# Kernel optimization log

Hardware: AMD Instinct MI355X
Metric: run time of the kernel (lower is better)

The kernel has to match this reference:

```python
import jax, jax.numpy as jnp
import numpy as np

B, S, N, SD = 1024, 8, 64, 36
EPS = 1e-5

def _lrelu(x):
    return jnp.where(x > 0, x, 0.01 * x)

def _inorm(x, g, b):
    # x: [B,S,N,C]; InstanceNorm(axis=3) on a [1,1,N,C] tensor normalizes over N per channel
    mu = jnp.mean(x, axis=2, keepdims=True)
    var = jnp.var(x, axis=2, keepdims=True)
    return (x - mu) * jax.lax.rsqrt(var + EPS) * g + b

def _conv1d_same(x, w, b):
    # x: [B,S,Cin], w: [K,Cin,Cout]; TF 'same' even-kernel pads (0, k-1-pl)
    k = w.shape[0]
    pl = (k - 1) // 2
    y = jax.lax.conv_general_dilated(x, w, (1,), [(pl, k - 1 - pl)],
                                     dimension_numbers=('NWC', 'WIO', 'NWC'))
    return y + b

def setup_inputs() -> dict:
    key = jax.random.key(0)
    ks = iter(jax.random.split(key, 64))
    d = {}
    d['fts'] = jax.random.normal(next(ks), (B, S, N, 5), jnp.float32)
    d['state'] = jax.random.normal(next(ks), (B, S, SD), jnp.float32)
    def w(shape, scale=0.05):
        return jax.random.normal(next(ks), shape, jnp.float32) * scale
    # pointnet (1x1 Conv2D == pointwise matmul)
    d['pw1'] = w((5, 32)); d['pb1'] = jnp.zeros((32,)); d['pg1'] = jnp.ones((32,)); d['pbe1'] = jnp.zeros((32,))
    d['pw2'] = w((32, 64)); d['pb2'] = jnp.zeros((64,)); d['pg2'] = jnp.ones((64,)); d['pbe2'] = jnp.zeros((64,))
    d['pw3'] = w((64, 128)); d['pb3'] = jnp.zeros((128,)); d['pg3'] = jnp.ones((128,)); d['pbe3'] = jnp.zeros((128,))
    d['pw4'] = w((128, 128)); d['pb4'] = jnp.zeros((128,))
    # fts_mergenet Conv1D stack + Dense
    d['mw1'] = w((2, 128, 128)); d['mb1'] = jnp.zeros((128,))
    d['mw2'] = w((2, 128, 64)); d['mb2'] = jnp.zeros((64,))
    d['mw3'] = w((2, 64, 64)); d['mb3'] = jnp.zeros((64,))
    d['mw4'] = w((2, 64, 64)); d['mb4'] = jnp.zeros((64,))
    d['mdw'] = w((S * 64, 128)); d['mdb'] = jnp.zeros((128,))
    # states_conv Conv1D stack + Dense
    d['sw1'] = w((2, SD, 128)); d['sb1'] = jnp.zeros((128,))
    d['sw2'] = w((2, 128, 64)); d['sb2'] = jnp.zeros((64,))
    d['sw3'] = w((2, 64, 64)); d['sb3'] = jnp.zeros((64,))
    d['sw4'] = w((2, 64, 64)); d['sb4'] = jnp.zeros((64,))
    d['sdw'] = w((S * 64, 128)); d['sdb'] = jnp.zeros((128,))
    # control module Dense stack
    d['cw1'] = w((256, 128)); d['cb1'] = jnp.zeros((128,))
    d['cw2'] = w((128, 64)); d['cb2'] = jnp.zeros((64,))
    d['cw3'] = w((64, 32)); d['cb3'] = jnp.zeros((32,))
    d['cw4'] = w((32, 4)); d['cb4'] = jnp.zeros((4,))
    return d

def reference(fts, state, pw1, pb1, pg1, pbe1, pw2, pb2, pg2, pbe2,
              pw3, pb3, pg3, pbe3, pw4, pb4,
              mw1, mb1, mw2, mb2, mw3, mb3, mw4, mb4, mdw, mdb,
              sw1, sb1, sw2, sb2, sw3, sb3, sw4, sb4, sdw, sdb,
              cw1, cb1, cw2, cb2, cw3, cb3, cw4, cb4):
    # --- pointnet, fully batched over (B,S) instead of tf.map_fn per timestep ---
    x = fts  # [B,S,N,5]
    x = _lrelu(_inorm(jnp.einsum('bsnc,cd->bsnd', x, pw1) + pb1, pg1, pbe1))
    x = _lrelu(_inorm(jnp.einsum('bsnc,cd->bsnd', x, pw2) + pb2, pg2, pbe2))
    x = _lrelu(_inorm(jnp.einsum('bsnc,cd->bsnd', x, pw3) + pb3, pg3, pbe3))
    x = jnp.einsum('bsnc,cd->bsnd', x, pw4) + pb4
    emb = jnp.mean(x, axis=2)  # GlobalAveragePooling2D over (1,N) -> [B,S,128]
    # --- fts_mergenet ---
    y = _lrelu(_conv1d_same(emb, mw1, mb1))
    y = _lrelu(_conv1d_same(y, mw2, mb2))
    y = _lrelu(_conv1d_same(y, mw3, mb3))
    y = _lrelu(_conv1d_same(y, mw4, mb4))
    fts_emb = y.reshape(y.shape[0], -1) @ mdw + mdb  # [B,128]
    # --- states branch ---
    z = _lrelu(_conv1d_same(state, sw1, sb1))
    z = _lrelu(_conv1d_same(z, sw2, sb2))
    z = _lrelu(_conv1d_same(z, sw3, sb3))
    z = _conv1d_same(z, sw4, sb4)  # no activation after 4th conv
    st_emb = z.reshape(z.shape[0], -1) @ sdw + sdb  # [B,128]
    # --- control head ---
    t = jnp.concatenate([fts_emb, st_emb], axis=1)  # [B,256]
    t = _lrelu(t @ cw1 + cb1)
    t = _lrelu(t @ cw2 + cb2)
    t = _lrelu(t @ cw3 + cb3)
    out = t @ cw4 + cb4  # [B,4]
    thrust = jax.nn.sigmoid(out[:, :1])
    body = jnp.tanh(out[:, 1:])
    mult = jnp.array([21.0, 6.0, 6.0, 6.0], dtype=out.dtype)
    return jnp.concatenate([thrust, body], axis=1) * mult
```

## Files before the change

kernel.cpp:

```cpp
#include <hip/hip_runtime.h>
#include <hip/hip_bf16.h>
#include <math.h>

#define THREADS 256

constexpr int S   = 8;
constexpr int NPT = 64;
constexpr int SD  = 36;
constexpr float EPS = 1e-5f;

typedef float v4f __attribute__((ext_vector_type(4)));
typedef __attribute__((ext_vector_type(8))) short bf8;
typedef __attribute__((ext_vector_type(4))) float f4;

__device__ __forceinline__ float lrelu(float x) { return fmaxf(x, 0.01f * x); }

__device__ __forceinline__ unsigned short f2bf(float x) {
  return __builtin_bit_cast(unsigned short, __float2bfloat16(x));
}

__device__ __forceinline__ void pack_frag(const float* __restrict__ src, unsigned short* __restrict__ dst,
                                          int slot, int NT, int TS, int CIN, int N) {
  const int f = slot >> 6, l = slot & 63;
  const int nt = f % NT, kt = f / NT;
  const int n = nt * 16 + (l & 15), g = (l >> 4);
  unsigned short* d = dst + (size_t)f * 512 + l * 8;
#pragma unroll
  for (int j = 0; j < 8; ++j) {
    int k = kt * 32 + g * 8 + j;
    float v;
    if (TS > 0) { int tap = k / TS, c = k - tap * TS; v = (c < CIN) ? src[(tap * CIN + c) * N + n] : 0.f; }
    else        v = (CIN == 0 || k < CIN) ? src[k * N + n] : 0.f;
    d[j] = f2bf(v);
  }
}

__device__ __forceinline__ void pack_frag_fold(const float* __restrict__ pw4,
    const float* __restrict__ mw1, unsigned short* __restrict__ dst, int slot) {
  const int f = slot >> 6, l = slot & 63;
  const int nt = f & 7, kt = f >> 3;
  const int n = nt * 16 + (l & 15), g = l >> 4;
  const int k0 = kt * 32 + g * 8;
  const int tap = k0 >> 7, c0 = k0 & 127;
  float acc[8] = {};
  const float* mcol = mw1 + (size_t)tap * 128 * 128 + n;
  const float* pr   = pw4 + (size_t)c0 * 128;
  for (int d = 0; d < 128; ++d) {
    float m = mcol[(size_t)d * 128];
#pragma unroll
    for (int j = 0; j < 8; ++j) acc[j] = fmaf(pr[j * 128 + d], m, acc[j]);
  }
  unsigned short* dd = dst + (size_t)f * 512 + l * 8;
#pragma unroll
  for (int j = 0; j < 8; ++j) dd[j] = f2bf(acc[j]);
}

#define WOFF_PNW1 0
#define WOFF_PNW2 1024
#define WOFF_PNW3 3072
#define WOFF_MW1  11264
#define WOFF_MW2  44032
#define WOFF_MW3  60416
#define WOFF_MW4  68608
#define WOFF_MDW  76800
#define WOFF_SW1  142336
#define WOFF_SW2  154624
#define WOFF_SW3  171008
#define WOFF_SW4  179200
#define WOFF_SDW  187392

__global__ void prep_weights(const float* __restrict__ pw1, const float* __restrict__ pw2,
    const float* __restrict__ pw3,
    const float* __restrict__ pw4, const float* __restrict__ pb4,
    const float* __restrict__ mw1, const float* __restrict__ mb1,
    const float* __restrict__ mw2, const float* __restrict__ mw3,
    const float* __restrict__ mw4, const float* __restrict__ mdw,
    const float* __restrict__ sw1, const float* __restrict__ sw2, const float* __restrict__ sw3,
    const float* __restrict__ sw4, const float* __restrict__ sdw,
    unsigned short* __restrict__ wf, float* __restrict__ mb1p, float* __restrict__ mb1p7) {
  const int slot = blockIdx.x * 256 + threadIdx.x;
  if      (slot <   128) pack_frag(pw1,    wf + WOFF_PNW1, slot,          2,   0,   5,  32);
  else if (slot <   384) pack_frag(pw2,    wf + WOFF_PNW2, slot - 128,    4,   0,   0,  64);
  else if (slot <  1408) pack_frag(pw3,    wf + WOFF_PNW3, slot - 384,    8,   0,   0, 128);
  else if (slot <  5504) pack_frag_fold(pw4, mw1, wf + WOFF_MW1, slot - 1408);
  else if (slot <  7552) pack_frag(mw2,    wf + WOFF_MW2,  slot - 5504,   4, 128, 128,  64);
  else if (slot <  8576) pack_frag(mw3,    wf + WOFF_MW3,  slot - 7552,   4,  64,  64,  64);
  else if (slot <  9600) pack_frag(mw4,    wf + WOFF_MW4,  slot - 8576,   4,  64,  64,  64);
  else if (slot < 17792) pack_frag(mdw,    wf + WOFF_MDW,  slot - 9600,   8,   0,   0, 128);
  else if (slot < 19328) pack_frag(sw1,    wf + WOFF_SW1,  slot - 17792,  8,  48,  36, 128);
  else if (slot < 21376) pack_frag(sw2,    wf + WOFF_SW2,  slot - 19328,  4, 128, 128,  64);
  else if (slot < 22400) pack_frag(sw3,    wf + WOFF_SW3,  slot - 21376,  4,  64,  64,  64);
  else if (slot < 23424) pack_frag(sw4,    wf + WOFF_SW4,  slot - 22400,  4,  64,  64,  64);
  else if (slot < 31616) pack_frag(sdw,    wf + WOFF_SDW,  slot - 23424,  8,   0,   0, 128);
  else if (slot < 31744) {
    const int n = slot - 31616;
    float a = mb1[n];
    for (int d = 0; d < 128; ++d)
      a = fmaf(pb4[d], mw1[(size_t)d * 128 + n] + mw1[(size_t)(128 + d) * 128 + n], a);
    mb1p[n] = a;
  } else if (slot < 31872) {
    const int n = slot - 31744;
    float a = mb1[n];
    for (int d = 0; d < 128; ++d) a = fmaf(pb4[d], mw1[(size_t)d * 128 + n], a);
    mb1p7[n] = a;
  }
}

__global__ __launch_bounds__(THREADS)
void pointnet_kernel(const float* __restrict__ fts,
    const unsigned short* __restrict__ w1f, const float* __restrict__ pg1, const float* __restrict__ pbe1,
    const unsigned short* __restrict__ w2f, const float* __restrict__ pg2, const float* __restrict__ pbe2,
    const unsigned short* __restrict__ w3f, const float* __restrict__ pg3, const float* __restrict__ pbe3,
    unsigned short* __restrict__ xbar_out)
{
  const int p = blockIdx.x;
  const int t = threadIdx.x;
  const int l = t & 63, w = t >> 6;
  const int g = l >> 4, lc = l & 15;

  __shared__ unsigned short xinb[64 * 40];
  __shared__ unsigned short x1b[64 * 40];
  __shared__ unsigned short x2b[64 * 72];

  {
    const float* src = fts + (size_t)p * 320;
    unsigned* xz = (unsigned*)xinb;
    const int row = t >> 2, cp = t & 3;
    const float* sr = src + row * 5;
    unsigned v0 = 0u;
    if (cp == 0)      v0 = (unsigned)f2bf(sr[0]) | ((unsigned)f2bf(sr[1]) << 16);
    else if (cp == 1) v0 = (unsigned)f2bf(sr[2]) | ((unsigned)f2bf(sr[3]) << 16);
    else if (cp == 2) v0 = (unsigned)f2bf(sr[4]);
    unsigned* xr = xz + row * 20;
    xr[cp]      = v0;
    xr[cp + 4]  = 0u;
    xr[cp + 8]  = 0u;
    xr[cp + 12] = 0u;
  }
  __syncthreads();

  if (w < 2) {
    f4 c1[4];
#pragma unroll
    for (int mt = 0; mt < 4; ++mt) c1[mt] = f4{0.f, 0.f, 0.f, 0.f};
    bf8 bfrag = *(const bf8*)(w1f + ((size_t)w * 64 + l) * 8);
#pragma unroll
    for (int mt = 0; mt < 4; ++mt) {
      bf8 afrag = *(const bf8*)(xinb + (mt * 16 + lc) * 40 + g * 8);
      c1[mt] = __builtin_amdgcn_mfma_f32_16x16x32_bf16(afrag, bfrag, c1[mt], 0, 0, 0);
    }
    float s = 0.f, q = 0.f;
#pragma unroll
    for (int mt = 0; mt < 4; ++mt)
#pragma unroll
      for (int r = 0; r < 4; ++r) { float v = c1[mt][r]; s += v; q = fmaf(v, v, q); }
    s += __shfl_xor(s, 16, 64); s += __shfl_xor(s, 32, 64);
    q += __shfl_xor(q, 16, 64); q += __shfl_xor(q, 32, 64);
    const int ch = w * 16 + lc;
    float mu  = s * (1.f / NPT);
    float inv = rsqrtf(q * (1.f / NPT) - mu * mu + EPS);
    float a = inv * pg1[ch];
    float bb = fmaf(-mu, a, pbe1[ch]);
#pragma unroll
    for (int mt = 0; mt < 4; ++mt)
#pragma unroll
      for (int r = 0; r < 4; ++r) {
        int row = mt * 16 + g * 4 + r;
        x1b[row * 40 + ch] = f2bf(lrelu(fmaf(c1[mt][r], a, bb)));
      }
  }
  __syncthreads();

  f4 c2[4];
#pragma unroll
  for (int mt = 0; mt < 4; ++mt) c2[mt] = f4{0.f, 0.f, 0.f, 0.f};
  {
    bf8 bfrag = *(const bf8*)(w2f + ((size_t)w * 64 + l) * 8);
#pragma unroll
    for (int mt = 0; mt < 4; ++mt) {
      bf8 afrag = *(const bf8*)(x1b + (mt * 16 + lc) * 40 + g * 8);
      c2[mt] = __builtin_amdgcn_mfma_f32_16x16x32_bf16(afrag, bfrag, c2[mt], 0, 0, 0);
    }
  }
  {
    float s = 0.f, q = 0.f;
#pragma unroll
    for (int mt = 0; mt < 4; ++mt)
#pragma unroll
      for (int r = 0; r < 4; ++r) { float v = c2[mt][r]; s += v; q = fmaf(v, v, q); }
    s += __shfl_xor(s, 16, 64); s += __shfl_xor(s, 32, 64);
    q += __shfl_xor(q, 16, 64); q += __shfl_xor(q, 32, 64);
    const int ch = w * 16 + lc;
    float mu  = s * (1.f / NPT);
    float inv = rsqrtf(q * (1.f / NPT) - mu * mu + EPS);
    float a = inv * pg2[ch];
    float bb = fmaf(-mu, a, pbe2[ch]);
#pragma unroll
    for (int mt = 0; mt < 4; ++mt)
#pragma unroll
      for (int r = 0; r < 4; ++r) {
        int row = mt * 16 + g * 4 + r;
        x2b[row * 72 + ch] = f2bf(lrelu(fmaf(c2[mt][r], a, bb)));
      }
  }
  __syncthreads();

  f4 c3[4][2];
#pragma unroll
  for (int mt = 0; mt < 4; ++mt)
#pragma unroll
    for (int n = 0; n < 2; ++n) c3[mt][n] = f4{0.f, 0.f, 0.f, 0.f};
  bf8 bf3[2][2];
#pragma unroll
  for (int ntl = 0; ntl < 2; ++ntl)
#pragma unroll
    for (int kt = 0; kt < 2; ++kt)
      bf3[ntl][kt] = *(const bf8*)(w3f + ((size_t)(kt * 8 + (2 * w + ntl)) * 64 + l) * 8);
#pragma unroll
  for (int mt = 0; mt < 4; ++mt)
#pragma unroll
    for (int kt = 0; kt < 2; ++kt) {
      bf8 afrag = *(const bf8*)(x2b + (mt * 16 + lc) * 72 + kt * 32 + g * 8);
#pragma unroll
      for (int ntl = 0; ntl < 2; ++ntl)
        c3[mt][ntl] = __builtin_amdgcn_mfma_f32_16x16x32_bf16(afrag, bf3[ntl][kt], c3[mt][ntl], 0, 0, 0);
    }

#pragma unroll
  for (int ntl = 0; ntl < 2; ++ntl) {
    float s = 0.f, q = 0.f;
#pragma unroll
    for (int mt = 0; mt < 4; ++mt)
#pragma unroll
      for (int r = 0; r < 4; ++r) { float v = c3[mt][ntl][r]; s += v; q = fmaf(v, v, q); }
    s += __shfl_xor(s, 16, 64); s += __shfl_xor(s, 32, 64);
    q += __shfl_xor(q, 16, 64); q += __shfl_xor(q, 32, 64);
    const int ch = w * 32 + ntl * 16 + lc;
    float mu  = s * (1.f / NPT);
    float inv = rsqrtf(q * (1.f / NPT) - mu * mu + EPS);
    float a = inv * pg3[ch];
    float bb = fmaf(-mu, a, pbe3[ch]);
    float m = 0.f;
#pragma unroll
    for (int mt = 0; mt < 4; ++mt)
#pragma unroll
      for (int r = 0; r < 4; ++r) m += lrelu(fmaf(c3[mt][ntl][r], a, bb));
    m += __shfl_xor(m, 16, 64); m += __shfl_xor(m, 32, 64);
    if (g == 0) xbar_out[(size_t)p * 128 + ch] = f2bf(m * (1.f / NPT));
  }
}

template<int KT, int NT, int TS, int SPI, int SPO, bool ACT>
__device__ __forceinline__ void mfma_conv(const unsigned short* __restrict__ xin,
    unsigned short* __restrict__ xout, const unsigned short* __restrict__ wfr,
    const float* __restrict__ bias, const float* __restrict__ bias7, int w, int l) {
  const int g = l >> 4, lc = l & 15;
  const int arow = w * 16 + lc, abl = arow >> 3, an = arow & 7;
  f4 acc[NT];
#pragma unroll
  for (int nt = 0; nt < NT; ++nt) acc[nt] = f4{0.f, 0.f, 0.f, 0.f};
#pragma unroll
  for (int kt = 0; kt < KT; ++kt) {
    const int k0 = kt * 32 + g * 8;
    const int tap = k0 / TS, c = k0 - tap * TS;
    bf8 a = *(const bf8*)(xin + (abl * 9 + an + tap) * SPI + c);
#pragma unroll
    for (int nt = 0; nt < NT; ++nt) {
      bf8 b = *(const bf8*)(wfr + ((size_t)(kt * NT + nt) * 64 + l) * 8);
      acc[nt] = __builtin_amdgcn_mfma_f32_16x16x32_bf16(a, b, acc[nt], 0, 0, 0);
    }
  }
  const int orow0 = w * 16 + g * 4;
#pragma unroll
  for (int nt = 0; nt < NT; ++nt) {
    const float bv  = bias[nt * 16 + lc];
    const float bv7 = bias7[nt * 16 + lc];
#pragma unroll
    for (int r = 0; r < 4; ++r) {
      const int rr = orow0 + r, obl = rr >> 3, on = rr & 7;
      float v = acc[nt][r] + (on == 7 ? bv7 : bv);
      if (ACT) v = lrelu(v);
      xout[(obl * 9 + on) * SPO + nt * 16 + lc] = f2bf(v);
    }
  }
}

__device__ __forceinline__ void mfma_dense512(const unsigned short* __restrict__ xin,
    float* __restrict__ P, const unsigned short* __restrict__ wfr, int w, int l) {
  const int g = l >> 4, lc = l & 15;
  const int bl = lc & 7;
  f4 acc[8];
#pragma unroll
  for (int nt = 0; nt < 8; ++nt) acc[nt] = f4{0.f, 0.f, 0.f, 0.f};
#pragma unroll
  for (int kt2 = 0; kt2 < 4; ++kt2) {
    const int kt = w * 4 + kt2;
    const int k0 = kt * 32 + g * 8;
    const int n = k0 >> 6, c = k0 & 63;
    bf8 a = *(const bf8*)(xin + (bl * 9 + n) * 72 + c);
#pragma unroll
    for (int nt = 0; nt < 8; ++nt) {
      bf8 b = *(const bf8*)(wfr + ((size_t)(kt * 8 + nt) * 64 + l) * 8);
      acc[nt] = __builtin_amdgcn_mfma_f32_16x16x32_bf16(a, b, acc[nt], 0, 0, 0);
    }
  }
  if (g < 2) {
#pragma unroll
    for (int nt = 0; nt < 8; ++nt)
#pragma unroll
      for (int r = 0; r < 4; ++r) {
        const int rr = g * 4 + r;
        P[(w * 8 + rr) * 128 + nt * 16 + lc] = acc[nt][r];
      }
  }
}

__global__ __launch_bounds__(THREADS)
void tail_mfma_kernel(const unsigned short* __restrict__ xbar, const float* __restrict__ state,
    const unsigned short* __restrict__ wf,
    const float* __restrict__ mb1p, const float* __restrict__ mb1p7,
    const float* __restrict__ mb2, const float* __restrict__ mb3,
    const float* __restrict__ mb4, const float* __restrict__ mdb,
    const float* __restrict__ sb1, const float* __restrict__ sb2, const float* __restrict__ sb3,
    const float* __restrict__ sb4, const float* __restrict__ sdb,
    float* __restrict__ femb, float* __restrict__ semb)
{
  const int t = threadIdx.x, l = t & 63, w = t >> 6;
  const bool merge = blockIdx.x < 128;
  const int bg = merge ? blockIdx.x : blockIdx.x - 128;

  __shared__ unsigned short lds[24768];
  unsigned short* BufX = lds;
  unsigned short* BufY = lds + 9792;
  unsigned short* BufZ = lds + 19584;

  { unsigned* z = (unsigned*)BufX; for (int i = t; i < 4896; i += THREADS) z[i] = 0; }
  for (int i = t; i < 8 * 136; i += THREADS) BufY[((i / 136) * 9 + 8) * 136 + (i % 136)] = 0;
  for (int i = t; i < 8 * 72;  i += THREADS) BufZ[((i / 72)  * 9 + 8) * 72  + (i % 72)]  = 0;

  if (merge) {
    for (int i = t; i < 1024; i += THREADS) {
      int bl = i >> 7, rem = i & 127, n = rem >> 4, sl = rem & 15;
      bf8 v = *(const bf8*)(xbar + (size_t)((bg * 8 + bl) * 8 + n) * 128 + sl * 8);
      *(bf8*)(BufX + (bl * 9 + n) * 136 + sl * 8) = v;
    }
  } else {
    for (int i = t; i < 2304; i += THREADS) {
      int bl = i / 288, rem = i % 288, n = rem / 36, c = rem % 36;
      BufX[(bl * 9 + n) * 48 + c] = f2bf(state[((size_t)(bg * 8 + bl) * 8 + n) * 36 + c]);
    }
  }
  __syncthreads();

  if (merge) mfma_conv<8, 8, 128, 136, 136, true>(BufX, BufY, wf + WOFF_MW1, mb1p, mb1p7, w, l);
  else       mfma_conv<3, 8,  48,  48, 136, true>(BufX, BufY, wf + WOFF_SW1, sb1, sb1, w, l);
  __syncthreads();
  if (merge) mfma_conv<8, 4, 128, 136, 72, true>(BufY, BufZ, wf + WOFF_MW2, mb2, mb2, w, l);
  else       mfma_conv<8, 4, 128, 136, 72, true>(BufY, BufZ, wf + WOFF_SW2, sb2, sb2, w, l);
  __syncthreads();
  for (int i = t; i < 8 * 72; i += THREADS) BufX[((i / 72) * 9 + 8) * 72 + (i % 72)] = 0;
  __syncthreads();
  if (merge) mfma_conv<4, 4, 64, 72, 72, true>(BufZ, BufX, wf + WOFF_MW3, mb3, mb3, w, l);
  else       mfma_conv<4, 4, 64, 72, 72, true>(BufZ, BufX, wf + WOFF_SW3, sb3, sb3, w, l);
  __syncthreads();
  if (merge) mfma_conv<4, 4, 64, 72, 72, true >(BufX, BufY, wf + WOFF_MW4, mb4, mb4, w, l);
  else       mfma_conv<4, 4, 64, 72, 72, false>(BufX, BufY, wf + WOFF_SW4, sb4, sb4, w, l);
  __syncthreads();

  float* P = (float*)lds;
  mfma_dense512(BufY, P, wf + (merge ? WOFF_MDW : WOFF_SDW), w, l);
  __syncthreads();

  const float* bias = merge ? mdb : sdb;
  float* outg = (merge ? femb : semb) + (size_t)bg * 1024;
  for (int i = t; i < 1024; i += THREADS) {
    int ch = i & 127, b = i >> 7;
    outg[i] = bias[ch] + P[(0 * 8 + b) * 128 + ch] + P[(1 * 8 + b) * 128 + ch]
                       + P[(2 * 8 + b) * 128 + ch] + P[(3 * 8 + b) * 128 + ch];
  }
}

template<int CIN, int COUT, bool ACT>
__device__ __forceinline__ void wave_dense(const float* __restrict__ in, float* __restrict__ out,
                                           const float* __restrict__ W, const float* __restrict__ bias, int l) {
  if constexpr (COUT >= 64) {
    constexpr int NC = COUT / 64;
    const int d0 = l * NC;
    float acc[NC];
#pragma unroll
    for (int k = 0; k < NC; ++k) acc[k] = bias[d0 + k];
#pragma unroll 4
    for (int c4 = 0; c4 < CIN / 4; ++c4) {
      v4f x4 = *(const v4f*)(in + 4 * c4);
#pragma unroll
      for (int j = 0; j < 4; ++j) {
        const float* wr = W + (4 * c4 + j) * COUT + d0;
#pragma unroll
        for (int k = 0; k < NC; ++k) acc[k] = fmaf(x4[j], wr[k], acc[k]);
      }
    }
#pragma unroll
    for (int k = 0; k < NC; ++k) out[d0 + k] = ACT ? lrelu(acc[k]) : acc[k];
  } else {
    if (l < COUT) {
      float acc = bias[l];
#pragma unroll 4
      for (int c4 = 0; c4 < CIN / 4; ++c4) {
        v4f x4 = *(const v4f*)(in + 4 * c4);
#pragma unroll
        for (int j = 0; j < 4; ++j) acc = fmaf(x4[j], W[(4 * c4 + j) * COUT + l], acc);
      }
      out[l] = ACT ? lrelu(acc) : acc;
    }
  }
}

__global__ __launch_bounds__(THREADS)
void head_kernel(const float* __restrict__ femb, const float* __restrict__ semb,
    const float* __restrict__ cw1, const float* __restrict__ cb1,
    const float* __restrict__ cw2, const float* __restrict__ cb2,
    const float* __restrict__ cw3, const float* __restrict__ cb3,
    const float* __restrict__ cw4, const float* __restrict__ cb4,
    float* __restrict__ out)
{
  const int t = threadIdx.x, l = t & 63, w = t >> 6;
  const int b = blockIdx.x * 4 + w;
  __shared__ float cat[4][256];
  __shared__ float hb[4][232];

  cat[w][l]       = femb[(size_t)b * 128 + l];
  cat[w][64 + l]  = femb[(size_t)b * 128 + 64 + l];
  cat[w][128 + l] = semb[(size_t)b * 128 + l];
  cat[w][192 + l] = semb[(size_t)b * 128 + 64 + l];
  __syncthreads();
  wave_dense<256, 128, true>(cat[w], hb[w], cw1, cb1, l);
  __syncthreads();
  wave_dense<128, 64, true>(hb[w], hb[w] + 128, cw2, cb2, l);
  __syncthreads();
  wave_dense<64, 32, true>(hb[w] + 128, hb[w] + 192, cw3, cb3, l);
  __syncthreads();
  if (l < 4) {
    float acc = cb4[l];
#pragma unroll
    for (int c = 0; c < 32; ++c) acc = fmaf(hb[w][192 + c], cw4[c * 4 + l], acc);
    out[(size_t)b * 4 + l] = (l == 0) ? 21.f / (1.f + expf(-acc)) : 6.f * tanhf(acc);
  }
}

extern "C" void kernel_launch(void* const* d_in, const int* in_sizes, int n_in,
                              void* d_out, int out_size, void* d_ws, size_t ws_size,
                              hipStream_t stream) {
  const float* p[44];
  for (int i = 0; i < 44; ++i) p[i] = (const float*)d_in[i];

  unsigned short* xbar_bf = (unsigned short*)d_ws;
  float* femb  = (float*)((char*)d_ws + 2097152);
  float* semb  = (float*)((char*)d_ws + 2621440);
  unsigned short* wf = (unsigned short*)((char*)d_ws + 3145728);
  float* mb1p  = (float*)((char*)d_ws + 3651584);
  float* mb1p7 = (float*)((char*)d_ws + 3652096);

  prep_weights<<<125, THREADS, 0, stream>>>(
      p[2], p[6], p[10],
      p[14], p[15], p[16], p[17],
      p[18], p[20], p[22], p[24],
      p[26], p[28], p[30], p[32], p[34],
      wf, mb1p, mb1p7);

  pointnet_kernel<<<1024 * S, THREADS, 0, stream>>>(
      p[0],
      wf + WOFF_PNW1, p[4], p[5],
      wf + WOFF_PNW2, p[8], p[9],
      wf + WOFF_PNW3, p[12], p[13],
      xbar_bf);

  tail_mfma_kernel<<<256, THREADS, 0, stream>>>(
      xbar_bf, p[1], wf,
      mb1p, mb1p7, p[19], p[21], p[23], p[25],
      p[27], p[29], p[31], p[33], p[35],
      femb, semb);

  head_kernel<<<256, THREADS, 0, stream>>>(
      femb, semb,
      p[36], p[37], p[38], p[39], p[40], p[41], p[42], p[43],
      (float*)d_out);
}
```

Before: 79.26 us.

## Fuse tail conv stacks with control head and hoist pointnet weight loads

```diff
diff --git a/kernel.cpp b/kernel.cpp
--- a/kernel.cpp
+++ b/kernel.cpp
@@ -43,12 +43,19 @@
   const int k0 = kt * 32 + g * 8;
   const int tap = k0 >> 7, c0 = k0 & 127;
   float acc[8] = {};
-  const float* mcol = mw1 + (size_t)tap * 128 * 128 + n;
-  const float* pr   = pw4 + (size_t)c0 * 128;
-  for (int d = 0; d < 128; ++d) {
-    float m = mcol[(size_t)d * 128];
-#pragma unroll
-    for (int j = 0; j < 8; ++j) acc[j] = fmaf(pr[j * 128 + d], m, acc[j]);
+  const float* mcol  = mw1 + (size_t)tap * 128 * 128 + n;
+  const float* pbase = pw4 + (size_t)c0 * 128;
+  for (int d4 = 0; d4 < 32; ++d4) {
+    const int d0 = 4 * d4;
+    float m0 = mcol[(size_t)(d0 + 0) * 128];
+    float m1 = mcol[(size_t)(d0 + 1) * 128];
+    float m2 = mcol[(size_t)(d0 + 2) * 128];
+    float m3 = mcol[(size_t)(d0 + 3) * 128];
+#pragma unroll
+    for (int j = 0; j < 8; ++j) {
+      v4f pv = *(const v4f*)(pbase + j * 128 + d0);
+      acc[j] = fmaf(pv[0], m0, fmaf(pv[1], m1, fmaf(pv[2], m2, fmaf(pv[3], m3, acc[j]))));
+    }
   }
   unsigned short* dd = dst + (size_t)f * 512 + l * 8;
 #pragma unroll
@@ -122,6 +129,16 @@
   __shared__ unsigned short x1b[64 * 40];
   __shared__ unsigned short x2b[64 * 72];
 
+  bf8 bfrag_w1 = {};
+  if (w < 2) bfrag_w1 = *(const bf8*)(w1f + ((size_t)w * 64 + l) * 8);
+  bf8 bfrag_w2 = *(const bf8*)(w2f + ((size_t)w * 64 + l) * 8);
+  bf8 bf3[2][2];
+#pragma unroll
+  for (int ntl = 0; ntl < 2; ++ntl)
+#pragma unroll
+    for (int kt = 0; kt < 2; ++kt)
+      bf3[ntl][kt] = *(const bf8*)(w3f + ((size_t)(kt * 8 + (2 * w + ntl)) * 64 + l) * 8);
+
   {
     const float* src = fts + (size_t)p * 320;
     unsigned* xz = (unsigned*)xinb;
@@ -143,11 +160,10 @@
     f4 c1[4];
 #pragma unroll
     for (int mt = 0; mt < 4; ++mt) c1[mt] = f4{0.f, 0.f, 0.f, 0.f};
-    bf8 bfrag = *(const bf8*)(w1f + ((size_t)w * 64 + l) * 8);
 #pragma unroll
     for (int mt = 0; mt < 4; ++mt) {
       bf8 afrag = *(const bf8*)(xinb + (mt * 16 + lc) * 40 + g * 8);
-      c1[mt] = __builtin_amdgcn_mfma_f32_16x16x32_bf16(afrag, bfrag, c1[mt], 0, 0, 0);
+      c1[mt] = __builtin_amdgcn_mfma_f32_16x16x32_bf16(afrag, bfrag_w1, c1[mt], 0, 0, 0);
     }
     float s = 0.f, q = 0.f;
 #pragma unroll
@@ -174,13 +190,10 @@
   f4 c2[4];
 #pragma unroll
   for (int mt = 0; mt < 4; ++mt) c2[mt] = f4{0.f, 0.f, 0.f, 0.f};
-  {
-    bf8 bfrag = *(const bf8*)(w2f + ((size_t)w * 64 + l) * 8);
-#pragma unroll
-    for (int mt = 0; mt < 4; ++mt) {
-      bf8 afrag = *(const bf8*)(x1b + (mt * 16 + lc) * 40 + g * 8);
-      c2[mt] = __builtin_amdgcn_mfma_f32_16x16x32_bf16(afrag, bfrag, c2[mt], 0, 0, 0);
-    }
+#pragma unroll
+  for (int mt = 0; mt < 4; ++mt) {
+    bf8 afrag = *(const bf8*)(x1b + (mt * 16 + lc) * 40 + g * 8);
+    c2[mt] = __builtin_amdgcn_mfma_f32_16x16x32_bf16(afrag, bfrag_w2, c2[mt], 0, 0, 0);
   }
   {
     float s = 0.f, q = 0.f;
@@ -210,12 +223,6 @@
   for (int mt = 0; mt < 4; ++mt)
 #pragma unroll
     for (int n = 0; n < 2; ++n) c3[mt][n] = f4{0.f, 0.f, 0.f, 0.f};
-  bf8 bf3[2][2];
-#pragma unroll
-  for (int ntl = 0; ntl < 2; ++ntl)
-#pragma unroll
-    for (int kt = 0; kt < 2; ++kt)
-      bf3[ntl][kt] = *(const bf8*)(w3f + ((size_t)(kt * 8 + (2 * w + ntl)) * 64 + l) * 8);
 #pragma unroll
   for (int mt = 0; mt < 4; ++mt)
 #pragma unroll
@@ -315,71 +322,6 @@
   }
 }
 
-__global__ __launch_bounds__(THREADS)
-void tail_mfma_kernel(const unsigned short* __restrict__ xbar, const float* __restrict__ state,
-    const unsigned short* __restrict__ wf,
-    const float* __restrict__ mb1p, const float* __restrict__ mb1p7,
-    const float* __restrict__ mb2, const float* __restrict__ mb3,
-    const float* __restrict__ mb4, const float* __restrict__ mdb,
-    const float* __restrict__ sb1, const float* __restrict__ sb2, const float* __restrict__ sb3,
-    const float* __restrict__ sb4, const float* __restrict__ sdb,
-    float* __restrict__ femb, float* __restrict__ semb)
-{
-  const int t = threadIdx.x, l = t & 63, w = t >> 6;
-  const bool merge = blockIdx.x < 128;
-  const int bg = merge ? blockIdx.x : blockIdx.x - 128;
-
-  __shared__ unsigned short lds[24768];
-  unsigned short* BufX = lds;
-  unsigned short* BufY = lds + 9792;
-  unsigned short* BufZ = lds + 19584;
-
-  { unsigned* z = (unsigned*)BufX; for (int i = t; i < 4896; i += THREADS) z[i] = 0; }
-  for (int i = t; i < 8 * 136; i += THREADS) BufY[((i / 136) * 9 + 8) * 136 + (i % 136)] = 0;
-  for (int i = t; i < 8 * 72;  i += THREADS) BufZ[((i / 72)  * 9 + 8) * 72  + (i % 72)]  = 0;
-
-  if (merge) {
-    for (int i = t; i < 1024; i += THREADS) {
-      int bl = i >> 7, rem = i & 127, n = rem >> 4, sl = rem & 15;
-      bf8 v = *(const bf8*)(xbar + (size_t)((bg * 8 + bl) * 8 + n) * 128 + sl * 8);
-      *(bf8*)(BufX + (bl * 9 + n) * 136 + sl * 8) = v;
-    }
-  } else {
-    for (int i = t; i < 2304; i += THREADS) {
-      int bl = i / 288, rem = i % 288, n = rem / 36, c = rem % 36;
-      BufX[(bl * 9 + n) * 48 + c] = f2bf(state[((size_t)(bg * 8 + bl) * 8 + n) * 36 + c]);
-    }
-  }
-  __syncthreads();
-
-  if (merge) mfma_conv<8, 8, 128, 136, 136, true>(BufX, BufY, wf + WOFF_MW1, mb1p, mb1p7, w, l);
-  else       mfma_conv<3, 8,  48,  48, 136, true>(BufX, BufY, wf + WOFF_SW1, sb1, sb1, w, l);
-  __syncthreads();
-  if (merge) mfma_conv<8, 4, 128, 136, 72, true>(BufY, BufZ, wf + WOFF_MW2, mb2, mb2, w, l);
-  else       mfma_conv<8, 4, 128, 136, 72, true>(BufY, BufZ, wf + WOFF_SW2, sb2, sb2, w, l);
-  __syncthreads();
-  for (int i = t; i < 8 * 72; i += THREADS) BufX[((i / 72) * 9 + 8) * 72 + (i % 72)] = 0;
-  __syncthreads();
-  if (merge) mfma_conv<4, 4, 64, 72, 72, true>(BufZ, BufX, wf + WOFF_MW3, mb3, mb3, w, l);
-  else       mfma_conv<4, 4, 64, 72, 72, true>(BufZ, BufX, wf + WOFF_SW3, sb3, sb3, w, l);
-  __syncthreads();
-  if (merge) mfma_conv<4, 4, 64, 72, 72, true >(BufX, BufY, wf + WOFF_MW4, mb4, mb4, w, l);
-  else       mfma_conv<4, 4, 64, 72, 72, false>(BufX, BufY, wf + WOFF_SW4, sb4, sb4, w, l);
-  __syncthreads();
-
-  float* P = (float*)lds;
-  mfma_dense512(BufY, P, wf + (merge ? WOFF_MDW : WOFF_SDW), w, l);
-  __syncthreads();
-
-  const float* bias = merge ? mdb : sdb;
-  float* outg = (merge ? femb : semb) + (size_t)bg * 1024;
-  for (int i = t; i < 1024; i += THREADS) {
-    int ch = i & 127, b = i >> 7;
-    outg[i] = bias[ch] + P[(0 * 8 + b) * 128 + ch] + P[(1 * 8 + b) * 128 + ch]
-                       + P[(2 * 8 + b) * 128 + ch] + P[(3 * 8 + b) * 128 + ch];
-  }
-}
-
 template<int CIN, int COUT, bool ACT>
 __device__ __forceinline__ void wave_dense(const float* __restrict__ in, float* __restrict__ out,
                                            const float* __restrict__ W, const float* __restrict__ bias, int l) {
@@ -415,8 +357,14 @@
   }
 }
 
-__global__ __launch_bounds__(THREADS)
-void head_kernel(const float* __restrict__ femb, const float* __restrict__ semb,
+__global__ __launch_bounds__(512)
+void tail_head_kernel(const unsigned short* __restrict__ xbar, const float* __restrict__ state,
+    const unsigned short* __restrict__ wf,
+    const float* __restrict__ mb1p, const float* __restrict__ mb1p7,
+    const float* __restrict__ mb2, const float* __restrict__ mb3,
+    const float* __restrict__ mb4, const float* __restrict__ mdb,
+    const float* __restrict__ sb1, const float* __restrict__ sb2, const float* __restrict__ sb3,
+    const float* __restrict__ sb4, const float* __restrict__ sdb,
     const float* __restrict__ cw1, const float* __restrict__ cb1,
     const float* __restrict__ cw2, const float* __restrict__ cb2,
     const float* __restrict__ cw3, const float* __restrict__ cb3,
@@ -424,25 +372,81 @@
     float* __restrict__ out)
 {
   const int t = threadIdx.x, l = t & 63, w = t >> 6;
-  const int b = blockIdx.x * 4 + w;
-  __shared__ float cat[4][256];
-  __shared__ float hb[4][232];
-
-  cat[w][l]       = femb[(size_t)b * 128 + l];
-  cat[w][64 + l]  = femb[(size_t)b * 128 + 64 + l];
-  cat[w][128 + l] = semb[(size_t)b * 128 + l];
-  cat[w][192 + l] = semb[(size_t)b * 128 + 64 + l];
-  __syncthreads();
-  wave_dense<256, 128, true>(cat[w], hb[w], cw1, cb1, l);
-  __syncthreads();
-  wave_dense<128, 64, true>(hb[w], hb[w] + 128, cw2, cb2, l);
-  __syncthreads();
-  wave_dense<64, 32, true>(hb[w] + 128, hb[w] + 192, cw3, cb3, l);
-  __syncthreads();
+  const int wl = w & 3;
+  const bool merge = w < 4;
+  const int tb = t & 255;
+  const int bg = blockIdx.x;
+
+  __shared__ unsigned short lds[2][24768];
+  unsigned short* base = lds[merge ? 0 : 1];
+  unsigned short* BufX = base;
+  unsigned short* BufY = base + 9792;
+  unsigned short* BufZ = base + 19584;
+
+  { unsigned* z = (unsigned*)BufX; for (int i = tb; i < 4896; i += 256) z[i] = 0; }
+  for (int i = tb; i < 8 * 136; i += 256) BufY[((i / 136) * 9 + 8) * 136 + (i % 136)] = 0;
+  for (int i = tb; i < 8 * 72;  i += 256) BufZ[((i / 72)  * 9 + 8) * 72  + (i % 72)]  = 0;
+
+  if (merge) {
+    for (int i = tb; i < 1024; i += 256) {
+      int bl = i >> 7, rem = i & 127, n = rem >> 4, sl = rem & 15;
+      bf8 v = *(const bf8*)(xbar + (size_t)((bg * 8 + bl) * 8 + n) * 128 + sl * 8);
+      *(bf8*)(BufX + (bl * 9 + n) * 136 + sl * 8) = v;
+    }
+  } else {
+    for (int i = tb; i < 2304; i += 256) {
+      int bl = i / 288, rem = i % 288, n = rem / 36, c = rem % 36;
+      BufX[(bl * 9 + n) * 48 + c] = f2bf(state[((size_t)(bg * 8 + bl) * 8 + n) * 36 + c]);
+    }
+  }
+  __syncthreads();
+
+  if (merge) mfma_conv<8, 8, 128, 136, 136, true>(BufX, BufY, wf + WOFF_MW1, mb1p, mb1p7, wl, l);
+  else       mfma_conv<3, 8,  48,  48, 136, true>(BufX, BufY, wf + WOFF_SW1, sb1, sb1, wl, l);
+  __syncthreads();
+  if (merge) mfma_conv<8, 4, 128, 136, 72, true>(BufY, BufZ, wf + WOFF_MW2, mb2, mb2, wl, l);
+  else       mfma_conv<8, 4, 128, 136, 72, true>(BufY, BufZ, wf + WOFF_SW2, sb2, sb2, wl, l);
+  __syncthreads();
+  for (int i = tb; i < 8 * 72; i += 256) BufX[((i / 72) * 9 + 8) * 72 + (i % 72)] = 0;
+  __syncthreads();
+  if (merge) mfma_conv<4, 4, 64, 72, 72, true>(BufZ, BufX, wf + WOFF_MW3, mb3, mb3, wl, l);
+  else       mfma_conv<4, 4, 64, 72, 72, true>(BufZ, BufX, wf + WOFF_SW3, sb3, sb3, wl, l);
+  __syncthreads();
+  if (merge) mfma_conv<4, 4, 64, 72, 72, true >(BufX, BufY, wf + WOFF_MW4, mb4, mb4, wl, l);
+  else       mfma_conv<4, 4, 64, 72, 72, false>(BufX, BufY, wf + WOFF_SW4, sb4, sb4, wl, l);
+  __syncthreads();
+
+  float* P = (float*)base;
+  mfma_dense512(BufY, P, wf + (merge ? WOFF_MDW : WOFF_SDW), wl, l);
+  __syncthreads();
+
+  float* P_m = (float*)lds[0];
+  float* P_s = (float*)lds[1];
+  float* cat = (float*)(lds[0] + 9792);
+  for (int i = t; i < 2048; i += 512) {
+    int b = i >> 8, c = i & 255;
+    float v;
+    if (c < 128)
+      v = mdb[c] + P_m[b * 128 + c] + P_m[(8 + b) * 128 + c]
+                 + P_m[(16 + b) * 128 + c] + P_m[(24 + b) * 128 + c];
+    else {
+      int ch = c & 127;
+      v = sdb[ch] + P_s[b * 128 + ch] + P_s[(8 + b) * 128 + ch]
+                  + P_s[(16 + b) * 128 + ch] + P_s[(24 + b) * 128 + ch];
+    }
+    cat[b * 256 + c] = v;
+  }
+  __syncthreads();
+
+  float* hb = (float*)(lds[1] + 9792) + w * 240;
+  wave_dense<256, 128, true>(cat + w * 256, hb, cw1, cb1, l);
+  wave_dense<128, 64, true>(hb, hb + 128, cw2, cb2, l);
+  wave_dense<64, 32, true>(hb + 128, hb + 192, cw3, cb3, l);
   if (l < 4) {
     float acc = cb4[l];
 #pragma unroll
-    for (int c = 0; c < 32; ++c) acc = fmaf(hb[w][192 + c], cw4[c * 4 + l], acc);
+    for (int c = 0; c < 32; ++c) acc = fmaf(hb[192 + c], cw4[c * 4 + l], acc);
+    const int b = bg * 8 + w;
     out[(size_t)b * 4 + l] = (l == 0) ? 21.f / (1.f + expf(-acc)) : 6.f * tanhf(acc);
   }
 }
@@ -454,11 +458,9 @@
   for (int i = 0; i < 44; ++i) p[i] = (const float*)d_in[i];
 
   unsigned short* xbar_bf = (unsigned short*)d_ws;
-  float* femb  = (float*)((char*)d_ws + 2097152);
-  float* semb  = (float*)((char*)d_ws + 2621440);
-  unsigned short* wf = (unsigned short*)((char*)d_ws + 3145728);
-  float* mb1p  = (float*)((char*)d_ws + 3651584);
-  float* mb1p7 = (float*)((char*)d_ws + 3652096);
+  unsigned short* wf = (unsigned short*)((char*)d_ws + 2097152);
+  float* mb1p  = (float*)((char*)d_ws + 2603008);
+  float* mb1p7 = (float*)((char*)d_ws + 2603520);
 
   prep_weights<<<125, THREADS, 0, stream>>>(
       p[2], p[6], p[10],
@@ -474,14 +476,10 @@
       wf + WOFF_PNW3, p[12], p[13],
       xbar_bf);
 
-  tail_mfma_kernel<<<256, THREADS, 0, stream>>>(
+  tail_head_kernel<<<128, 512, 0, stream>>>(
       xbar_bf, p[1], wf,
       mb1p, mb1p7, p[19], p[21], p[23], p[25],
       p[27], p[29], p[31], p[33], p[35],
-      femb, semb);
-
-  head_kernel<<<256, THREADS, 0, stream>>>(
-      femb, semb,
       p[36], p[37], p[38], p[39], p[40], p[41], p[42], p[43],
       (float*)d_out);
 }
```

New measurement: 91.32 us. 1.15x slower.
